# Kernel optimization log

Measured on AMD Instinct MI355X. Metric: run time of the kernel, lower is better.

Reference implementation:

```python
import jax, jax.numpy as jnp
import numpy as np
from jax import lax

EPS = 1e-5
K = 3            # FreqFilter kernel size
G = 8            # groups = out_ch // channel_per_group = 64 // 8


def conv2d(x, w, pad):
    return lax.conv_general_dilated(
        x, w, window_strides=(1, 1), padding=[(pad, pad), (pad, pad)],
        dimension_numbers=("NCHW", "OIHW", "NCHW"))


def leaky(x):
    return jnp.where(x >= 0, x, 0.01 * x)


def freq_filter(y, wf, gamma, beta):
    # y: (n, c, h, w) with c = 64
    n, c, h, w = y.shape
    yp = jnp.pad(y, ((0, 0), (0, 0), (1, 1), (1, 1)), mode="reflect")
    sig = conv2d(yp, wf, pad=0)                       # (n, G*K*K, h, w)
    # BatchNorm2d in training mode: batch statistics over (N,H,W)
    mu = sig.mean(axis=(0, 2, 3), keepdims=True)
    var = sig.var(axis=(0, 2, 3), keepdims=True)
    sig = (sig - mu) * lax.rsqrt(var + EPS)
    sig = sig * gamma[None, :, None, None] + beta[None, :, None, None]
    sig = jax.nn.softmax(sig, axis=1)                 # softmax over all G*K*K channels
    sig = sig.reshape(n, G, K * K, h, w)              # channel = g*(K*K) + k
    # kernel = identity (delta at center tap) - sigma
    center = K * K // 2
    delta = jnp.zeros((K * K,), sig.dtype).at[center].set(1.0)
    kernel = delta[None, None, :, None, None] - sig   # (n, G, 9, h, w)
    # im2col patches of the reflect-padded input, unfold ordering (row-major taps)
    patches = jnp.stack(
        [yp[:, :, i:i + h, j:j + w] for i in range(K) for j in range(K)],
        axis=2)                                        # (n, c, 9, h, w)
    patches = patches.reshape(n, G, c // G, K * K, h, w)
    out = jnp.einsum("ngckhw,ngkhw->ngchw", patches, kernel)
    return out.reshape(n, c, h, w)


def hin(x):
    # InstanceNorm2d (affine=False) on first half of channels
    half = x.shape[1] // 2
    a = x[:, :half]
    mu = a.mean(axis=(2, 3), keepdims=True)
    var = a.var(axis=(2, 3), keepdims=True)
    a = (a - mu) * lax.rsqrt(var + EPS)
    return jnp.concatenate([a, x[:, half:]], axis=1)


def setup_inputs() -> dict:
    key = jax.random.key(0)
    ks = jax.random.split(key, 8)
    n, cin, cout, h, w = 4, 64, 64, 256, 256
    return {
        "x": jax.random.normal(ks[0], (n, cin, h, w), jnp.float32),
        "w1": jax.random.normal(ks[1], (cout, cin, 3, 3), jnp.float32) * 0.05,
        "b1": jax.random.normal(ks[2], (cout,), jnp.float32) * 0.01,
        "wf": jax.random.normal(ks[3], (G * K * K, cout, 3, 3), jnp.float32) * 0.06,
        "bn_gamma": jnp.ones((G * K * K,), jnp.float32),
        "bn_beta": jnp.zeros((G * K * K,), jnp.float32),
        "w2": jax.random.normal(ks[4], (cout, cout, 3, 3), jnp.float32) * 0.05,
        "b2": jax.random.normal(ks[5], (cout,), jnp.float32) * 0.01,
        "wr": jax.random.normal(ks[6], (cout, cin, 1, 1), jnp.float32) * 0.1,
        "br": jax.random.normal(ks[7], (cout,), jnp.float32) * 0.01,
    }


def reference(x, w1, b1, wf, bn_gamma, bn_beta, w2, b2, wr, br):
    y = conv2d(x, w1, pad=1) + b1[None, :, None, None]
    y = freq_filter(y, wf, bn_gamma, bn_beta)
    y = leaky(hin(y))
    y = leaky(conv2d(y, w2, pad=1) + b2[None, :, None, None])
    res = conv2d(x, wr, pad=0) + br[None, :, None, None]
    return res + y
```

## Files before the change

kernel.cpp:

```cpp
#include <hip/hip_runtime.h>

typedef unsigned short u16;
typedef __attribute__((ext_vector_type(8))) short bf16x8;
typedef __attribute__((ext_vector_type(4))) float f32x4;
typedef __attribute__((address_space(3))) void lds_void;
typedef __attribute__((address_space(1))) const void gbl_void;

#define NN 4
#define HH 256
#define WW 256
#define PD 258
#define CIN 64
#define EPSV 1e-5f

__device__ __forceinline__ float b2f(u16 x){ union{unsigned u; float f;} q; q.u = ((unsigned)x)<<16; return q.f; }
__device__ __forceinline__ u16 f2b(float f){ union{float f; unsigned u;} q; q.f = f; unsigned r = q.u + 0x7FFF + ((q.u>>16)&1u); return (u16)(r>>16); }
__device__ __forceinline__ float leakyf(float x){ return x >= 0.f ? x : 0.01f*x; }

__global__ void prep_kernel(const float* __restrict__ w1, const float* __restrict__ wf,
                            const float* __restrict__ w2, const float* __restrict__ wr,
                            u16* __restrict__ wB1, u16* __restrict__ wBf,
                            u16* __restrict__ wB2, u16* __restrict__ wBr){
  int idx = blockIdx.x*256 + threadIdx.x;
  if (idx < 36864){
    int e = idx & 7, lane = (idx >> 3) & 63, q = idx >> 9;
    int f = q & 3, ksq = q >> 2, ks = ksq & 1, tap = ksq >> 1;
    int cout = f*16 + (lane & 15);
    int cin  = ks*32 + (lane >> 4)*8 + e;
    wB1[idx] = f2b(w1[(cout*64 + cin)*9 + tap]);
    wB2[idx] = f2b(w2[(cout*64 + cin)*9 + tap]);
  }
  if (idx < 46080){
    int e = idx & 7, lane = (idx >> 3) & 63, q = idx >> 9;
    int f = q % 5, ksq = q / 5, ks = ksq & 1, tap = ksq >> 1;
    int cout = f*16 + (lane & 15);
    int cin  = ks*32 + (lane >> 4)*8 + e;
    float v = (cout < 72) ? wf[(cout*64 + cin)*9 + tap] : 0.f;
    wBf[idx] = f2b(v);
  }
  if (idx < 4096){
    int e = idx & 7, lane = (idx >> 3) & 63, q = idx >> 9;
    int f = q & 3, ks = q >> 2;
    int cout = f*16 + (lane & 15);
    int cin  = ks*32 + (lane >> 4)*8 + e;
    wBr[idx] = f2b(wr[cout*64 + cin]);
  }
}

__global__ __launch_bounds__(256) void padx_kernel(const float* __restrict__ x, u16* __restrict__ xpad){
  int n = blockIdx.x >> 8, h = blockIdx.x & 255, t = threadIdx.x;
  u16* dstrow = xpad + ((size_t)(n*PD + h + 1)*PD)*CIN;
  const uint4 z = {0,0,0,0};
  #pragma unroll
  for (int c8 = 0; c8 < 8; ++c8){
    u16 buf[8];
    #pragma unroll
    for (int j = 0; j < 8; ++j)
      buf[j] = f2b(x[((size_t)(n*64 + c8*8 + j))*65536 + h*256 + t]);
    *(uint4*)(dstrow + (size_t)(t+1)*CIN + c8*8) = *(uint4*)buf;
  }
  if (t == 0)   { for (int c8 = 0; c8 < 8; ++c8) *(uint4*)(dstrow + 0*CIN   + c8*8) = z; }
  if (t == 255) { for (int c8 = 0; c8 < 8; ++c8) *(uint4*)(dstrow + 257*CIN + c8*8) = z; }
  if (h == 0 || h == 255){
    u16* brow = xpad + ((size_t)(n*PD + (h == 0 ? 0 : 257))*PD)*CIN;
    for (int p = t; p < PD; p += 256)
      for (int c8 = 0; c8 < 8; ++c8) *(uint4*)(brow + (size_t)p*CIN + c8*8) = z;
  }
}

__global__ void reflect_kernel(u16* __restrict__ y1pad){
  int idx = blockIdx.x*256 + threadIdx.x;
  if (idx >= 4*1028*8) return;
  int n = idx/(1028*8), rem = idx%(1028*8), p = rem >> 3, cc = rem & 7;
  int pr, pc;
  if      (p < 258)  { pr = 0;   pc = p; }
  else if (p < 516)  { pr = 257; pc = p - 258; }
  else if (p < 772)  { pr = 1 + (p - 516); pc = 0; }
  else               { pr = 1 + (p - 772); pc = 257; }
  int sr = (pr == 0) ? 2 : ((pr == 257) ? 255 : pr);
  int sc = (pc == 0) ? 2 : ((pc == 257) ? 255 : pc);
  uint4 v = *(const uint4*)(y1pad + ((size_t)(n*PD + sr)*PD + sc)*CIN + cc*8);
  *(uint4*)(y1pad + ((size_t)(n*PD + pr)*PD + pc)*CIN + cc*8) = v;
}

template<int NF, int MODE>
__global__ __launch_bounds__(256, 3) void conv_mfma(
    const u16* __restrict__ Ain, const u16* __restrict__ wB, const float* __restrict__ bias,
    u16* __restrict__ outB, float* __restrict__ outF,
    const u16* __restrict__ xpad, const u16* __restrict__ wBr,
    const float* __restrict__ br,
    float* __restrict__ bnsum, float* __restrict__ bnsumsq){

  constexpr int NC  = NF*16;
  constexpr int NCP = NC + 8;
  __shared__ __align__(16) char smem[3328*16];

  int t = threadIdx.x, lane = t & 63, wv = t >> 6;
  int bid = blockIdx.x;
  int sb = (bid & 7)*256 + (bid >> 3);
  int n = sb >> 9, r = sb & 511, h = r >> 1, wt = r & 1, w0 = wt*128;
  int l15 = lane & 15, l4 = lane >> 4;
  const int pc0 = w0 + wv*32 + l15;

  {
    const u16* base = Ain + ((size_t)(n*PD + h)*PD + w0)*CIN;
    #pragma unroll
    for (int rnd = 0; rnd < 13; ++rnd){
      int c_d = rnd*256 + wv*64 + lane;
      int c = (c_d < 3120) ? c_d : 3119;
      int row = (c >= 2080) ? 2 : ((c >= 1040) ? 1 : 0);
      int rem = c - row*1040;
      int px = rem >> 3, sub = rem & 7;
      int subs = sub ^ (px & 7);
      const u16* src = base + (size_t)row*PD*CIN + (size_t)(px*8 + subs)*8;
      __builtin_amdgcn_global_load_lds((gbl_void*)src,
                                       (lds_void*)(smem + (rnd*256 + wv*64)*16), 16, 0, 0);
    }
  }
  __syncthreads();

  f32x4 acc[2][NF];
  #pragma unroll
  for (int mf = 0; mf < 2; ++mf)
    #pragma unroll
    for (int f = 0; f < NF; ++f) acc[mf][f] = (f32x4){0.f,0.f,0.f,0.f};

  #pragma unroll
  for (int tap = 0; tap < 9; ++tap){
    const int dh = tap/3, dw = tap%3;
    #pragma unroll
    for (int ks = 0; ks < 2; ++ks){
      bf16x8 wfr[NF];
      #pragma unroll
      for (int f = 0; f < NF; ++f)
        wfr[f] = *(const bf16x8*)(wB + ((size_t)(((tap*2 + ks)*NF + f)*64 + lane))*8);
      #pragma unroll
      for (int mf = 0; mf < 2; ++mf){
        int px = wv*32 + mf*16 + l15 + dw;
        int j  = ks*4 + l4;
        bf16x8 afr = *(const bf16x8*)(smem + ((((dh*130 + px) << 3) + (j ^ (px & 7))) << 4));
        #pragma unroll
        for (int f = 0; f < NF; ++f)
          acc[mf][f] = __builtin_amdgcn_mfma_f32_16x16x32_bf16(afr, wfr[f], acc[mf][f], 0, 0, 0);
      }
    }
  }

  if (MODE < 2){
    __syncthreads();
    u16* Bx = (u16*)smem;
    float* bnpart = (float*)(smem + 24576);
    if (MODE == 1){
      #pragma unroll
      for (int f = 0; f < NF; ++f){
        float s = 0.f, q = 0.f;
        #pragma unroll
        for (int mf = 0; mf < 2; ++mf)
          #pragma unroll
          for (int reg = 0; reg < 4; ++reg){ float v = acc[mf][f][reg]; s += v; q += v*v; }
        s += __shfl_xor(s, 16); q += __shfl_xor(q, 16);
        s += __shfl_xor(s, 32); q += __shfl_xor(q, 32);
        if (l4 == 0){
          bnpart[((wv*NF + f)*16 + l15)*2 + 0] = s;
          bnpart[((wv*NF + f)*16 + l15)*2 + 1] = q;
        }
      }
    }
    #pragma unroll
    for (int mf = 0; mf < 2; ++mf)
      #pragma unroll
      for (int f = 0; f < NF; ++f){
        int cout = f*16 + l15;
        float bv = (MODE == 0) ? bias[cout] : 0.f;
        #pragma unroll
        for (int reg = 0; reg < 4; ++reg){
          int px = wv*32 + mf*16 + l4*4 + reg;
          Bx[px*NCP + cout] = f2b(acc[mf][f][reg] + bv);
        }
      }
    __syncthreads();
    const int nch = NC/8;
    for (int idx = t; idx < 128*nch; idx += 256){
      int px = idx/nch, c8 = idx - px*nch;
      uint4 v = *(const uint4*)(Bx + px*NCP + c8*8);
      if (MODE == 0)
        *(uint4*)(outB + ((size_t)(n*PD + h + 1)*PD + (w0 + 1 + px))*CIN + c8*8) = v;
      else
        *(uint4*)(outB + ((size_t)(n*65536 + h*256 + w0 + px))*80 + c8*8) = v;
    }
    if (MODE == 1 && t < 160){
      int c = t >> 1, which = t & 1;
      if (c < 72){
        int fi = c >> 4, li = c & 15;
        float v = bnpart[((0*NF + fi)*16 + li)*2 + which] + bnpart[((1*NF + fi)*16 + li)*2 + which]
                + bnpart[((2*NF + fi)*16 + li)*2 + which] + bnpart[((3*NF + fi)*16 + li)*2 + which];
        atomicAdd(which ? &bnsumsq[c] : &bnsum[c], v);
      }
    }
  } else {
    const u16* Xn = xpad + ((size_t)(n*PD + h + 1)*PD + 1)*CIN;
    #pragma unroll
    for (int mf = 0; mf < 2; ++mf){
      bf16x8 xf0 = *(const bf16x8*)(Xn + (size_t)(pc0 + mf*16)*CIN + l4*8);
      bf16x8 xf1 = *(const bf16x8*)(Xn + (size_t)(pc0 + mf*16)*CIN + 32 + l4*8);
      #pragma unroll
      for (int f = 0; f < NF; ++f){
        int cout = f*16 + l15;
        bf16x8 b0 = *(const bf16x8*)(wBr + ((size_t)((0*NF + f)*64 + lane))*8);
        bf16x8 b1 = *(const bf16x8*)(wBr + ((size_t)((1*NF + f)*64 + lane))*8);
        f32x4 tmp = (f32x4){0.f,0.f,0.f,0.f};
        tmp = __builtin_amdgcn_mfma_f32_16x16x32_bf16(xf0, b0, tmp, 0, 0, 0);
        tmp = __builtin_amdgcn_mfma_f32_16x16x32_bf16(xf1, b1, tmp, 0, 0, 0);
        float bv = bias[cout], bb = br[cout];
        float4 o;
        o.x = leakyf(acc[mf][f][0] + bv) + tmp[0] + bb;
        o.y = leakyf(acc[mf][f][1] + bv) + tmp[1] + bb;
        o.z = leakyf(acc[mf][f][2] + bv) + tmp[2] + bb;
        o.w = leakyf(acc[mf][f][3] + bv) + tmp[3] + bb;
        int px = wv*32 + mf*16 + l4*4;
        *(float4*)(outF + ((size_t)(n*64 + cout))*65536 + h*256 + w0 + px) = o;
      }
    }
  }
}

__global__ void bnfinal_kernel(const float* __restrict__ bnsum, const float* __restrict__ bnsumsq,
                               const float* __restrict__ gamma, const float* __restrict__ beta,
                               float* __restrict__ bnscale, float* __restrict__ bnshift){
  int c = threadIdx.x;
  if (c < 72){
    const float M = 262144.f;
    float mu  = bnsum[c] / M;
    float var = bnsumsq[c] / M - mu*mu;
    float sc  = gamma[c] * rsqrtf(var + EPSV);
    bnscale[c] = sc;
    bnshift[c] = beta[c] - mu*sc;
  }
}

__global__ __launch_bounds__(256, 3) void filter_kernel(const u16* __restrict__ sig,
                                                        const u16* __restrict__ y1pad,
                                                        const float* __restrict__ bnscale,
                                                        const float* __restrict__ bnshift,
                                                        u16* __restrict__ y2pad,
                                                        float* __restrict__ hinsum,
                                                        float* __restrict__ hinsumsq){
  __shared__ __align__(16) char smem[3328*16];
  float* ps = (float*)(smem + 49920);
  __shared__ float sc[72], sh[72];

  int t = threadIdx.x, lane = t & 63, wv = t >> 6;
  if (t < 72){ sc[t] = bnscale[t]; sh[t] = bnshift[t]; }
  int bid = blockIdx.x;
  int sb = (bid & 7)*256 + (bid >> 3);
  int n = sb >> 9, r = sb & 511, h = r >> 1, wt = r & 1, w0 = wt*128;
  int px = t & 127, half = t >> 7;

  {
    const u16* base = y1pad + ((size_t)(n*PD + h)*PD + w0)*CIN;
    #pragma unroll
    for (int rnd = 0; rnd < 13; ++rnd){
      int c_d = rnd*256 + wv*64 + lane;
      int c = (c_d < 3120) ? c_d : 3119;
      int row = (c >= 2080) ? 2 : ((c >= 1040) ? 1 : 0);
      int rem = c - row*1040;
      int wpx = rem >> 3, sub = rem & 7;
      int subs = sub ^ (wpx & 7);
      const u16* src = base + (size_t)row*PD*CIN + (size_t)(wpx*8 + subs)*8;
      __builtin_amdgcn_global_load_lds((gbl_void*)src,
                                       (lds_void*)(smem + (rnd*256 + wv*64)*16), 16, 0, 0);
    }
  }

  float sv[72];
  const u16* sp = sig + ((size_t)(n*65536 + h*256 + w0 + px))*80;
  #pragma unroll
  for (int i = 0; i < 9; ++i){
    uint4 v = *(const uint4*)(sp + i*8);
    const u16* e = (const u16*)&v;
    #pragma unroll
    for (int j = 0; j < 8; ++j) sv[i*8+j] = b2f(e[j]);
  }
  __syncthreads();
  float mx = -1e30f;
  #pragma unroll
  for (int c = 0; c < 72; ++c){ sv[c] = sv[c]*sc[c] + sh[c]; mx = fmaxf(mx, sv[c]); }
  float sum = 0.f;
  #pragma unroll
  for (int c = 0; c < 72; ++c){ sv[c] = __expf(sv[c] - mx); sum += sv[c]; }
  float inv = -1.f/sum;
  float kv[36];
  if (half == 0){
    #pragma unroll
    for (int j = 0; j < 36; ++j) kv[j] = sv[j]*inv;
  } else {
    #pragma unroll
    for (int j = 0; j < 36; ++j) kv[j] = sv[36 + j]*inv;
  }
  #pragma unroll
  for (int c8 = 0; c8 < 4; ++c8) kv[c8*9 + 4] += 1.f;

  float o[32];
  #pragma unroll
  for (int c = 0; c < 32; ++c) o[c] = 0.f;
  #pragma unroll
  for (int i = 0; i < 3; ++i){
    #pragma unroll
    for (int j = 0; j < 3; ++j){
      int wpx = px + j;
      #pragma unroll
      for (int c8 = 0; c8 < 4; ++c8){
        int chunk = half*4 + c8;
        uint4 v = *(const uint4*)(smem + ((((i*130 + wpx) << 3) + (chunk ^ (wpx & 7))) << 4));
        const u16* e = (const u16*)&v;
        float k = kv[c8*9 + i*3 + j];
        #pragma unroll
        for (int jj = 0; jj < 8; ++jj) o[c8*8 + jj] = fmaf(k, b2f(e[jj]), o[c8*8 + jj]);
      }
    }
  }
  __syncthreads();

  u16* obuf = (u16*)smem;
  #pragma unroll
  for (int c8 = 0; c8 < 4; ++c8){
    u16 ob[8];
    #pragma unroll
    for (int jj = 0; jj < 8; ++jj) ob[jj] = f2b(o[c8*8 + jj]);
    *(uint4*)(obuf + px*66 + (half*4 + c8)*8) = *(uint4*)ob;
  }
  __syncthreads();

  {
    int c = t & 31, seg = t >> 5;
    float s = 0.f, q = 0.f;
    #pragma unroll
    for (int rr = 0; rr < 16; ++rr){
      float v = b2f(obuf[(seg*16 + rr)*66 + c]);
      s += v; q += v*v;
    }
    ps[(seg*32 + c)*2 + 0] = s; ps[(seg*32 + c)*2 + 1] = q;
  }
  u16* wrow = y2pad + ((size_t)(n*PD + h + 1)*PD + w0 + 1)*CIN;
  for (int idx = t; idx < 1024; idx += 256){
    int p = idx >> 3, j = idx & 7;
    uint4 v = *(const uint4*)(obuf + p*66 + j*8);
    *(uint4*)(wrow + (size_t)p*CIN + j*8) = v;
  }
  __syncthreads();
  if (t < 64){
    int c = t >> 1, which = t & 1;
    float v = 0.f;
    #pragma unroll
    for (int seg = 0; seg < 8; ++seg) v += ps[(seg*32 + c)*2 + which];
    atomicAdd(which ? &hinsumsq[n*32 + c] : &hinsum[n*32 + c], v);
  }
}

__global__ void hinfinal_kernel(const float* __restrict__ hinsum, const float* __restrict__ hinsumsq,
                                float* __restrict__ hmu, float* __restrict__ hrs){
  int i = threadIdx.x;
  if (i < 128){
    const float M = 65536.f;
    float mu  = hinsum[i] / M;
    float var = hinsumsq[i] / M - mu*mu;
    hmu[i] = mu;
    hrs[i] = rsqrtf(var + EPSV);
  }
}

__global__ __launch_bounds__(256) void hinapply_kernel(u16* __restrict__ y2pad,
                                                       const float* __restrict__ hmu,
                                                       const float* __restrict__ hrs){
  int n = blockIdx.x / PD, pr = blockIdx.x % PD, t = threadIdx.x;
  u16* row = y2pad + (size_t)(n*PD + pr)*PD*CIN;
  bool ringrow = (pr == 0) || (pr == PD-1);
  for (int idx = t; idx < PD*8; idx += 256){
    int px = idx >> 3, cc = idx & 7;
    uint4* p = (uint4*)(row + (size_t)px*CIN + cc*8);
    if (ringrow || px == 0 || px == PD-1){
      uint4 z = {0,0,0,0}; *p = z; continue;
    }
    uint4 v = *p;
    u16* e = (u16*)&v;
    if (cc < 4){
      int cb = n*32 + cc*8;
      #pragma unroll
      for (int j = 0; j < 8; ++j){
        float f = (b2f(e[j]) - hmu[cb+j]) * hrs[cb+j];
        e[j] = f2b(leakyf(f));
      }
    } else {
      #pragma unroll
      for (int j = 0; j < 8; ++j) e[j] = f2b(leakyf(b2f(e[j])));
    }
    *p = v;
  }
}

extern "C" void kernel_launch(void* const* d_in, const int* in_sizes, int n_in,
                              void* d_out, int out_size, void* d_ws, size_t ws_size,
                              hipStream_t stream){
  const float* x     = (const float*)d_in[0];
  const float* w1    = (const float*)d_in[1];
  const float* b1    = (const float*)d_in[2];
  const float* wf    = (const float*)d_in[3];
  const float* gamma = (const float*)d_in[4];
  const float* beta  = (const float*)d_in[5];
  const float* w2    = (const float*)d_in[6];
  const float* b2    = (const float*)d_in[7];
  const float* wr    = (const float*)d_in[8];
  const float* br    = (const float*)d_in[9];

  char* ws = (char*)d_ws;
  const size_t PADB = (size_t)NN*PD*PD*CIN*2;
  u16* xpad  = (u16*)(ws);
  u16* y1pad = (u16*)(ws + PADB);
  u16* y2pad = (u16*)(ws + 2*PADB);
  float* stats = (float*)(ws + 3*PADB);
  float* bnsum   = stats;        float* bnsumsq = stats + 80;
  float* bnscale = stats + 160;  float* bnshift = stats + 240;
  float* hinsum  = stats + 320;  float* hinsumsq= stats + 448;
  float* hmu     = stats + 576;  float* hrs     = stats + 704;
  u16* wB1 = (u16*)(ws + 3*PADB + 4096);
  u16* wBf = wB1 + 36864;
  u16* wB2 = wBf + 46080;
  u16* wBr = wB2 + 36864;

  u16* sig = (u16*)d_out;
  float* out = (float*)d_out;

  hipMemsetAsync(stats, 0, 4096, stream);
  prep_kernel<<<180, 256, 0, stream>>>(w1, wf, w2, wr, wB1, wBf, wB2, wBr);
  padx_kernel<<<NN*HH, 256, 0, stream>>>(x, xpad);
  conv_mfma<4,0><<<2048, 256, 0, stream>>>(xpad, wB1, b1, y1pad, nullptr, nullptr, nullptr, nullptr, nullptr, nullptr);
  reflect_kernel<<<(4*1028*8 + 255)/256, 256, 0, stream>>>(y1pad);
  conv_mfma<5,1><<<2048, 256, 0, stream>>>(y1pad, wBf, nullptr, sig, nullptr, nullptr, nullptr, nullptr, bnsum, bnsumsq);
  bnfinal_kernel<<<1, 80, 0, stream>>>(bnsum, bnsumsq, gamma, beta, bnscale, bnshift);
  filter_kernel<<<2048, 256, 0, stream>>>(sig, y1pad, bnscale, bnshift, y2pad, hinsum, hinsumsq);
  hinfinal_kernel<<<1, 128, 0, stream>>>(hinsum, hinsumsq, hmu, hrs);
  hinapply_kernel<<<NN*PD, 256, 0, stream>>>(y2pad, hmu, hrs);
  conv_mfma<4,2><<<2048, 256, 0, stream>>>(y2pad, wB2, b2, nullptr, out, xpad, wBr, br, nullptr, nullptr);
}
```

Measured before the change: 236.8 us.

## Retile conv and filter blocks to 2x64 pixel tiles to cut halo LDS

Each block of the conv and filter kernels now covers 2 rows by 64 columns instead of 1 row by 128 columns. The input halo staged in LDS shrinks from 3 rows by 130 pixels to 4 rows by 66 pixels, which lowers shared memory per block. Launch bounds rise from 3 to 4 blocks per SIMD to use the freed LDS for higher occupancy. The trade-offs are more redundant halo columns per output pixel, shorter contiguous global write runs, and tighter register limits from the occupancy hint, which could cause spills.

```diff
diff --git a/kernel.cpp b/kernel.cpp
--- a/kernel.cpp
+++ b/kernel.cpp
@@ -84,7 +84,7 @@
 }
 
 template<int NF, int MODE>
-__global__ __launch_bounds__(256, 3) void conv_mfma(
+__global__ __launch_bounds__(256, 4) void conv_mfma(
     const u16* __restrict__ Ain, const u16* __restrict__ wB, const float* __restrict__ bias,
     u16* __restrict__ outB, float* __restrict__ outF,
     const u16* __restrict__ xpad, const u16* __restrict__ wBr,
@@ -93,28 +93,29 @@
 
   constexpr int NC  = NF*16;
   constexpr int NCP = NC + 8;
-  __shared__ __align__(16) char smem[3328*16];
+  __shared__ __align__(16) char smem[2112*16];
 
   int t = threadIdx.x, lane = t & 63, wv = t >> 6;
   int bid = blockIdx.x;
   int sb = (bid & 7)*256 + (bid >> 3);
-  int n = sb >> 9, r = sb & 511, h = r >> 1, wt = r & 1, w0 = wt*128;
+  int n = sb >> 9, rem = sb & 511, rowb = rem >> 2, colb = rem & 3;
+  int h0 = rowb*2, w0 = colb*64;
   int l15 = lane & 15, l4 = lane >> 4;
-  const int pc0 = w0 + wv*32 + l15;
+  int r = wv >> 1, ch = wv & 1;
 
   {
-    const u16* base = Ain + ((size_t)(n*PD + h)*PD + w0)*CIN;
-    #pragma unroll
-    for (int rnd = 0; rnd < 13; ++rnd){
-      int c_d = rnd*256 + wv*64 + lane;
-      int c = (c_d < 3120) ? c_d : 3119;
-      int row = (c >= 2080) ? 2 : ((c >= 1040) ? 1 : 0);
-      int rem = c - row*1040;
-      int px = rem >> 3, sub = rem & 7;
-      int subs = sub ^ (px & 7);
-      const u16* src = base + (size_t)row*PD*CIN + (size_t)(px*8 + subs)*8;
-      __builtin_amdgcn_global_load_lds((gbl_void*)src,
-                                       (lds_void*)(smem + (rnd*256 + wv*64)*16), 16, 0, 0);
+    const u16* base = Ain + ((size_t)(n*PD + h0)*PD + w0)*CIN;
+    #pragma unroll
+    for (int rnd = 0; rnd < 9; ++rnd){
+      if (rnd < 8 || wv == 0){
+        int c = rnd*256 + wv*64 + lane;
+        int row = c / 528, rem2 = c - row*528;
+        int px = rem2 >> 3, sub = rem2 & 7;
+        int subs = sub ^ (px & 7);
+        const u16* src = base + (size_t)row*PD*CIN + (size_t)(px*8 + subs)*8;
+        __builtin_amdgcn_global_load_lds((gbl_void*)src,
+                                         (lds_void*)(smem + (rnd*256 + wv*64)*16), 16, 0, 0);
+      }
     }
   }
   __syncthreads();
@@ -136,9 +137,10 @@
         wfr[f] = *(const bf16x8*)(wB + ((size_t)(((tap*2 + ks)*NF + f)*64 + lane))*8);
       #pragma unroll
       for (int mf = 0; mf < 2; ++mf){
-        int px = wv*32 + mf*16 + l15 + dw;
+        int wcol = ch*32 + mf*16 + l15 + dw;
+        int wrow = r + dh;
         int j  = ks*4 + l4;
-        bf16x8 afr = *(const bf16x8*)(smem + ((((dh*130 + px) << 3) + (j ^ (px & 7))) << 4));
+        bf16x8 afr = *(const bf16x8*)(smem + ((((wrow*66 + wcol) << 3) + (j ^ (wcol & 7))) << 4));
         #pragma unroll
         for (int f = 0; f < NF; ++f)
           acc[mf][f] = __builtin_amdgcn_mfma_f32_16x16x32_bf16(afr, wfr[f], acc[mf][f], 0, 0, 0);
@@ -174,7 +176,7 @@
         float bv = (MODE == 0) ? bias[cout] : 0.f;
         #pragma unroll
         for (int reg = 0; reg < 4; ++reg){
-          int px = wv*32 + mf*16 + l4*4 + reg;
+          int px = r*64 + ch*32 + mf*16 + l4*4 + reg;
           Bx[px*NCP + cout] = f2b(acc[mf][f][reg] + bv);
         }
       }
@@ -182,11 +184,12 @@
     const int nch = NC/8;
     for (int idx = t; idx < 128*nch; idx += 256){
       int px = idx/nch, c8 = idx - px*nch;
+      int rr = px >> 6, cc = px & 63;
       uint4 v = *(const uint4*)(Bx + px*NCP + c8*8);
       if (MODE == 0)
-        *(uint4*)(outB + ((size_t)(n*PD + h + 1)*PD + (w0 + 1 + px))*CIN + c8*8) = v;
+        *(uint4*)(outB + ((size_t)(n*PD + h0 + 1 + rr)*PD + (w0 + 1 + cc))*CIN + c8*8) = v;
       else
-        *(uint4*)(outB + ((size_t)(n*65536 + h*256 + w0 + px))*80 + c8*8) = v;
+        *(uint4*)(outB + ((size_t)(n*65536 + (h0 + rr)*256 + w0 + cc))*80 + c8*8) = v;
     }
     if (MODE == 1 && t < 160){
       int c = t >> 1, which = t & 1;
@@ -198,11 +201,12 @@
       }
     }
   } else {
-    const u16* Xn = xpad + ((size_t)(n*PD + h + 1)*PD + 1)*CIN;
+    const u16* Xn = xpad + ((size_t)(n*PD + h0 + 1 + r)*PD + w0 + 1)*CIN;
     #pragma unroll
     for (int mf = 0; mf < 2; ++mf){
-      bf16x8 xf0 = *(const bf16x8*)(Xn + (size_t)(pc0 + mf*16)*CIN + l4*8);
-      bf16x8 xf1 = *(const bf16x8*)(Xn + (size_t)(pc0 + mf*16)*CIN + 32 + l4*8);
+      int pxc = ch*32 + mf*16 + l15;
+      bf16x8 xf0 = *(const bf16x8*)(Xn + (size_t)pxc*CIN + l4*8);
+      bf16x8 xf1 = *(const bf16x8*)(Xn + (size_t)pxc*CIN + 32 + l4*8);
       #pragma unroll
       for (int f = 0; f < NF; ++f){
         int cout = f*16 + l15;
@@ -217,8 +221,8 @@
         o.y = leakyf(acc[mf][f][1] + bv) + tmp[1] + bb;
         o.z = leakyf(acc[mf][f][2] + bv) + tmp[2] + bb;
         o.w = leakyf(acc[mf][f][3] + bv) + tmp[3] + bb;
-        int px = wv*32 + mf*16 + l4*4;
-        *(float4*)(outF + ((size_t)(n*64 + cout))*65536 + h*256 + w0 + px) = o;
+        int px = ch*32 + mf*16 + l4*4;
+        *(float4*)(outF + ((size_t)(n*64 + cout))*65536 + (h0 + r)*256 + w0 + px) = o;
       }
     }
   }
@@ -238,42 +242,42 @@
   }
 }
 
-__global__ __launch_bounds__(256, 3) void filter_kernel(const u16* __restrict__ sig,
+__global__ __launch_bounds__(256, 4) void filter_kernel(const u16* __restrict__ sig,
                                                         const u16* __restrict__ y1pad,
                                                         const float* __restrict__ bnscale,
                                                         const float* __restrict__ bnshift,
                                                         u16* __restrict__ y2pad,
                                                         float* __restrict__ hinsum,
                                                         float* __restrict__ hinsumsq){
-  __shared__ __align__(16) char smem[3328*16];
-  float* ps = (float*)(smem + 49920);
+  __shared__ __align__(16) char smem[2112*16];
   __shared__ float sc[72], sh[72];
 
   int t = threadIdx.x, lane = t & 63, wv = t >> 6;
   if (t < 72){ sc[t] = bnscale[t]; sh[t] = bnshift[t]; }
   int bid = blockIdx.x;
   int sb = (bid & 7)*256 + (bid >> 3);
-  int n = sb >> 9, r = sb & 511, h = r >> 1, wt = r & 1, w0 = wt*128;
-  int px = t & 127, half = t >> 7;
+  int n = sb >> 9, rem = sb & 511, rowb = rem >> 2, colb = rem & 3;
+  int h0 = rowb*2, w0 = colb*64;
+  int p = t & 127, r = p >> 6, c = p & 63, half = t >> 7;
 
   {
-    const u16* base = y1pad + ((size_t)(n*PD + h)*PD + w0)*CIN;
-    #pragma unroll
-    for (int rnd = 0; rnd < 13; ++rnd){
-      int c_d = rnd*256 + wv*64 + lane;
-      int c = (c_d < 3120) ? c_d : 3119;
-      int row = (c >= 2080) ? 2 : ((c >= 1040) ? 1 : 0);
-      int rem = c - row*1040;
-      int wpx = rem >> 3, sub = rem & 7;
-      int subs = sub ^ (wpx & 7);
-      const u16* src = base + (size_t)row*PD*CIN + (size_t)(wpx*8 + subs)*8;
-      __builtin_amdgcn_global_load_lds((gbl_void*)src,
-                                       (lds_void*)(smem + (rnd*256 + wv*64)*16), 16, 0, 0);
+    const u16* base = y1pad + ((size_t)(n*PD + h0)*PD + w0)*CIN;
+    #pragma unroll
+    for (int rnd = 0; rnd < 9; ++rnd){
+      if (rnd < 8 || wv == 0){
+        int cch = rnd*256 + wv*64 + lane;
+        int row = cch / 528, rem2 = cch - row*528;
+        int px = rem2 >> 3, sub = rem2 & 7;
+        int subs = sub ^ (px & 7);
+        const u16* src = base + (size_t)row*PD*CIN + (size_t)(px*8 + subs)*8;
+        __builtin_amdgcn_global_load_lds((gbl_void*)src,
+                                         (lds_void*)(smem + (rnd*256 + wv*64)*16), 16, 0, 0);
+      }
     }
   }
 
   float sv[72];
-  const u16* sp = sig + ((size_t)(n*65536 + h*256 + w0 + px))*80;
+  const u16* sp = sig + ((size_t)(n*65536 + (h0 + r)*256 + w0 + c))*80;
   #pragma unroll
   for (int i = 0; i < 9; ++i){
     uint4 v = *(const uint4*)(sp + i*8);
@@ -284,10 +288,10 @@
   __syncthreads();
   float mx = -1e30f;
   #pragma unroll
-  for (int c = 0; c < 72; ++c){ sv[c] = sv[c]*sc[c] + sh[c]; mx = fmaxf(mx, sv[c]); }
+  for (int cc = 0; cc < 72; ++cc){ sv[cc] = sv[cc]*sc[cc] + sh[cc]; mx = fmaxf(mx, sv[cc]); }
   float sum = 0.f;
   #pragma unroll
-  for (int c = 0; c < 72; ++c){ sv[c] = __expf(sv[c] - mx); sum += sv[c]; }
+  for (int cc = 0; cc < 72; ++cc){ sv[cc] = __expf(sv[cc] - mx); sum += sv[cc]; }
   float inv = -1.f/sum;
   float kv[36];
   if (half == 0){
@@ -302,16 +306,16 @@
 
   float o[32];
   #pragma unroll
-  for (int c = 0; c < 32; ++c) o[c] = 0.f;
+  for (int cc = 0; cc < 32; ++cc) o[cc] = 0.f;
   #pragma unroll
   for (int i = 0; i < 3; ++i){
     #pragma unroll
     for (int j = 0; j < 3; ++j){
-      int wpx = px + j;
+      int wcol = c + j, wrow = r + i;
       #pragma unroll
       for (int c8 = 0; c8 < 4; ++c8){
         int chunk = half*4 + c8;
-        uint4 v = *(const uint4*)(smem + ((((i*130 + wpx) << 3) + (chunk ^ (wpx & 7))) << 4));
+        uint4 v = *(const uint4*)(smem + ((((wrow*66 + wcol) << 3) + (chunk ^ (wcol & 7))) << 4));
         const u16* e = (const u16*)&v;
         float k = kv[c8*9 + i*3 + j];
         #pragma unroll
@@ -322,38 +326,39 @@
   __syncthreads();
 
   u16* obuf = (u16*)smem;
+  float* ps = (float*)(smem + 20480);
   #pragma unroll
   for (int c8 = 0; c8 < 4; ++c8){
     u16 ob[8];
     #pragma unroll
     for (int jj = 0; jj < 8; ++jj) ob[jj] = f2b(o[c8*8 + jj]);
-    *(uint4*)(obuf + px*66 + (half*4 + c8)*8) = *(uint4*)ob;
+    *(uint4*)(obuf + p*66 + (half*4 + c8)*8) = *(uint4*)ob;
   }
   __syncthreads();
 
   {
-    int c = t & 31, seg = t >> 5;
+    int cch = t & 31, seg = t >> 5;
     float s = 0.f, q = 0.f;
     #pragma unroll
     for (int rr = 0; rr < 16; ++rr){
-      float v = b2f(obuf[(seg*16 + rr)*66 + c]);
+      float v = b2f(obuf[(seg*16 + rr)*66 + cch]);
       s += v; q += v*v;
     }
-    ps[(seg*32 + c)*2 + 0] = s; ps[(seg*32 + c)*2 + 1] = q;
-  }
-  u16* wrow = y2pad + ((size_t)(n*PD + h + 1)*PD + w0 + 1)*CIN;
+    ps[(seg*32 + cch)*2 + 0] = s; ps[(seg*32 + cch)*2 + 1] = q;
+  }
   for (int idx = t; idx < 1024; idx += 256){
-    int p = idx >> 3, j = idx & 7;
-    uint4 v = *(const uint4*)(obuf + p*66 + j*8);
-    *(uint4*)(wrow + (size_t)p*CIN + j*8) = v;
+    int pp = idx >> 3, j = idx & 7;
+    int rr = pp >> 6, cc = pp & 63;
+    uint4 v = *(const uint4*)(obuf + pp*66 + j*8);
+    *(uint4*)(y2pad + ((size_t)(n*PD + h0 + 1 + rr)*PD + (w0 + 1 + cc))*CIN + j*8) = v;
   }
   __syncthreads();
   if (t < 64){
-    int c = t >> 1, which = t & 1;
+    int cc = t >> 1, which = t & 1;
     float v = 0.f;
     #pragma unroll
-    for (int seg = 0; seg < 8; ++seg) v += ps[(seg*32 + c)*2 + which];
-    atomicAdd(which ? &hinsumsq[n*32 + c] : &hinsum[n*32 + c], v);
+    for (int seg = 0; seg < 8; ++seg) v += ps[(seg*32 + cc)*2 + which];
+    atomicAdd(which ? &hinsumsq[n*32 + cc] : &hinsum[n*32 + cc], v);
   }
 }
 
```

Measured after the change: 228.5 us. 1.04x faster.
